# Kernel optimization log

Measured on AMD Instinct MI355X. Metric: run time of the kernel, lower is better.

Reference implementation:

```python
import jax, jax.numpy as jnp
import numpy as np
from jax import lax

DN = ('NCHW', 'OIHW', 'NCHW')


def _conv(x, w):
    # Conv2d(k=3, stride=2, padding=1, bias=False)
    return lax.conv_general_dilated(x, w, (2, 2), [(1, 1), (1, 1)], dimension_numbers=DN)


def _deconv(x, w):
    # ConvTranspose2d(k=3, stride=2, padding=1, output_padding=1, bias=False)
    # == input dilation 2 with asymmetric pad (k-1-p, k-1-p+output_padding) = (1, 2)
    return lax.conv_general_dilated(x, w, (1, 1), [(1, 2), (1, 2)], lhs_dilation=(2, 2), dimension_numbers=DN)


def _vq(z, codebook):
    B, C, H, W = z.shape
    z_flat = jnp.transpose(z, (0, 2, 3, 1)).reshape(-1, C)  # [BHW, C]
    dist = (jnp.sum(z_flat * z_flat, axis=1, keepdims=True)
            - 2.0 * z_flat @ codebook.T
            + jnp.sum(codebook * codebook, axis=1)[None, :])  # [BHW, K]
    ids = jnp.argmin(dist, axis=1)  # [BHW]
    e_k = codebook[ids]  # [BHW, C]
    e_k_st = z_flat + lax.stop_gradient(e_k - z_flat)
    e_k = jnp.transpose(e_k.reshape(B, H, W, C), (0, 3, 1, 2))
    e_k_st = jnp.transpose(e_k_st.reshape(B, H, W, C), (0, 3, 1, 2))
    return e_k, e_k_st, ids.reshape(B, H, W)


def _forward(x, enc_w0, enc_w1, enc_w2, codebook, dec_w0, dec_w1, dec_w2):
    # encoder
    h = jax.nn.relu(_conv(x, enc_w0))
    h = jax.nn.relu(_conv(h, enc_w1))
    z = _conv(h, enc_w2)  # no relu on last encoder layer
    # vector quantize
    e_k, e_k_st, ids = _vq(z, codebook)
    # decoder
    d = jax.nn.relu(_deconv(e_k_st, dec_w0))
    d = jax.nn.relu(_deconv(d, dec_w1))
    out = jax.nn.sigmoid(_deconv(d, dec_w2))
    return out, z, e_k, ids


def setup_inputs() -> dict:
    key = jax.random.key(0)
    ks = jax.random.split(key, 8)
    fan = lambda s: 1.0 / np.sqrt(np.prod(s[1:]))
    K = 1024
    return {
        'x': jax.random.uniform(ks[0], (32, 3, 256, 256), dtype=jnp.float32),
        'enc_w0': jax.random.normal(ks[1], (64, 3, 3, 3), jnp.float32) * fan((64, 3, 3, 3)),
        'enc_w1': jax.random.normal(ks[2], (128, 64, 3, 3), jnp.float32) * fan((128, 64, 3, 3)),
        'enc_w2': jax.random.normal(ks[3], (256, 128, 3, 3), jnp.float32) * fan((256, 128, 3, 3)),
        'codebook': jax.random.uniform(ks[4], (K, 256), jnp.float32, -1.0 / K, 1.0 / K),
        'dec_w0': jax.random.normal(ks[5], (128, 256, 3, 3), jnp.float32) * fan((128, 256, 3, 3)),
        'dec_w1': jax.random.normal(ks[6], (64, 128, 3, 3), jnp.float32) * fan((64, 128, 3, 3)),
        'dec_w2': jax.random.normal(ks[7], (3, 64, 3, 3), jnp.float32) * fan((3, 64, 3, 3)),
    }


def reference(x, enc_w0, enc_w1, enc_w2, codebook, dec_w0, dec_w1, dec_w2):
    return _forward(x, enc_w0, enc_w1, enc_w2, codebook, dec_w0, dec_w1, dec_w2)
```

## Files before the change

### kernel.cpp

```cpp
#include <hip/hip_runtime.h>
#include <math.h>


__global__ __launch_bounds__(256) void pad_zero_k(float* __restrict__ buf,
                                                  int HP, int WP) {
  float* p = buf + (size_t)blockIdx.x * HP * WP;
  const int tid = threadIdx.x;
  if (tid < WP) p[tid] = 0.f;
  if (tid >= 1 && tid < HP) p[(size_t)tid * WP] = 0.f;
}

template <int CIN, int COB, int PY, int LX, int MINW, int ACT>
__global__ __launch_bounds__(256, MINW) void conv3x3_s2_py(
    const float* __restrict__ in, const float* __restrict__ wgt,
    float* __restrict__ out, int COUT, int HIN, int WIN, int tilesW,
    int OHP, int OWP, int po) {
  const int HOUT = HIN >> 1, WOUT = WIN >> 1;
  const int YG = 256 / LX;
  const int tid = threadIdx.x;
  const int x = (blockIdx.x % tilesW) * LX + (tid % LX);
  const int y0 = (blockIdx.x / tilesW) * (YG * PY) + (tid / LX) * PY;
  const int co0 = blockIdx.y * COB;
  const int n = blockIdx.z;
  if (x >= WOUT || y0 >= HOUT) return;

  float acc[COB][PY], sum[COB][PY];
#pragma unroll
  for (int c = 0; c < COB; ++c)
#pragma unroll
    for (int r = 0; r < PY; ++r) { acc[c][r] = 0.f; sum[c][r] = 0.f; }

  const int ix0 = 2 * x - 1;
  const int iy0 = 2 * y0 - 1;
  for (int ci = 0; ci < CIN; ++ci) {
    const float* ip = in + (size_t)(n * CIN + ci) * HIN * WIN;
    float v[2 * PY + 1][3];
#pragma unroll
    for (int j = 0; j < 2 * PY + 1; ++j) {
      const int iy = iy0 + j;
      const bool yok = (unsigned)iy < (unsigned)HIN;
#pragma unroll
      for (int kx = 0; kx < 3; ++kx) {
        const int ix = ix0 + kx;
        v[j][kx] =
            (yok && (unsigned)ix < (unsigned)WIN) ? ip[iy * WIN + ix] : 0.f;
      }
    }
#pragma unroll
    for (int t = 0; t < 9; ++t) {
      const int kk = ci * 9 + t;
      if (CIN * 9 > 384 && (kk == 384 || kk == 768)) {
#pragma unroll
        for (int c = 0; c < COB; ++c)
#pragma unroll
          for (int r = 0; r < PY; ++r) {
            sum[c][r] = sum[c][r] + acc[c][r];
            acc[c][r] = 0.f;
          }
      }
      const int ky = t / 3, kx = t % 3;
#pragma unroll
      for (int c = 0; c < COB; ++c) {
        const float w = wgt[((size_t)(co0 + c) * CIN + ci) * 9 + t];
#pragma unroll
        for (int r = 0; r < PY; ++r)
          acc[c][r] = fmaf(v[2 * r + ky][kx], w, acc[c][r]);
      }
    }
  }
#pragma unroll
  for (int c = 0; c < COB; ++c)
#pragma unroll
    for (int r = 0; r < PY; ++r) {
      if (y0 + r < HOUT) {
        float rv = sum[c][r] + acc[c][r];
        if (ACT == 1) rv = fmaxf(rv, 0.f);
        out[(((size_t)n * COUT + co0 + c) * OHP + y0 + r + po) * OWP + x + po] =
            rv;
      }
    }
}

template <int CIN, int COB, int PY, int LX, int WINL, int MINW, int ACT,
          int PO>
__global__ __launch_bounds__(256, MINW) void conv3x3_s2_pad(
    const float* __restrict__ in, const float* __restrict__ wgt,
    float* __restrict__ out, int COUT, int tilesW) {
  constexpr int WP = WINL + 1;
  constexpr int HP = WINL + 1;
  constexpr size_t planeP = (size_t)HP * WP;
  constexpr int HOUT = WINL >> 1, WOUT = WINL >> 1;
  constexpr int OWP = WOUT + PO;
  constexpr int OHP = HOUT + PO;
  const int YG = 256 / LX;
  const int tid = threadIdx.x;
  const int x = (blockIdx.x % tilesW) * LX + (tid % LX);
  const int y0 = (blockIdx.x / tilesW) * (YG * PY) + (tid / LX) * PY;
  const int co0 = blockIdx.y * COB;
  const int n = blockIdx.z;
  if (x >= WOUT || y0 >= HOUT) return;

  float acc[COB][PY], sum[COB][PY];
#pragma unroll
  for (int c = 0; c < COB; ++c)
#pragma unroll
    for (int r = 0; r < PY; ++r) { acc[c][r] = 0.f; sum[c][r] = 0.f; }

  const float* bp = in + (size_t)(n * CIN) * planeP + (size_t)(2 * y0) * WP +
                    2 * x;
  for (int ci = 0; ci < CIN; ++ci, bp += planeP) {
    float v[2 * PY + 1][3];
#pragma unroll
    for (int j = 0; j < 2 * PY + 1; ++j)
#pragma unroll
      for (int kx = 0; kx < 3; ++kx) v[j][kx] = bp[j * WP + kx];
#pragma unroll
    for (int t = 0; t < 9; ++t) {
      const int kk = ci * 9 + t;
      if (CIN * 9 > 384 && (kk == 384 || kk == 768)) {
#pragma unroll
        for (int c = 0; c < COB; ++c)
#pragma unroll
          for (int r = 0; r < PY; ++r) {
            sum[c][r] = sum[c][r] + acc[c][r];
            acc[c][r] = 0.f;
          }
      }
      const int ky = t / 3, kx = t % 3;
#pragma unroll
      for (int c = 0; c < COB; ++c) {
        const float w = wgt[((size_t)(co0 + c) * CIN + ci) * 9 + t];
#pragma unroll
        for (int r = 0; r < PY; ++r)
          acc[c][r] = fmaf(v[2 * r + ky][kx], w, acc[c][r]);
      }
    }
  }
#pragma unroll
  for (int c = 0; c < COB; ++c)
#pragma unroll
    for (int r = 0; r < PY; ++r) {
      float rv = sum[c][r] + acc[c][r];
      if (ACT == 1) rv = fmaxf(rv, 0.f);
      out[(((size_t)n * COUT + co0 + c) * OHP + y0 + r + PO) * OWP + x + PO] =
          rv;
    }
}

template <int CIN, int COB, int MINW, int ACT>
__global__ __launch_bounds__(256, MINW) void deconv3x3_s2_quad2(
    const float* __restrict__ in, const float* __restrict__ wgt,
    float* __restrict__ out, int COUT, int HIN, int WIN, int tilesW) {
  const int HOUT = HIN * 2, WOUT = WIN * 2;
  const int tid = threadIdx.x;
  const int mx0 = ((blockIdx.x % tilesW) * 16 + (tid & 15)) * 2;
  const int my = (blockIdx.x / tilesW) * 16 + (tid >> 4);
  const int co0 = blockIdx.y * COB;
  const int n = blockIdx.z;
  if (mx0 >= WIN || my >= HIN) return;
  const bool xe = (mx0 + 2 < WIN);
  const bool ye = (my + 1 < HIN);

  float accA[COB][4], accB[COB][4];
#pragma unroll
  for (int c = 0; c < COB; ++c)
#pragma unroll
    for (int q = 0; q < 4; ++q) { accA[c][q] = 0.f; accB[c][q] = 0.f; }

  const size_t plane = (size_t)HIN * WIN;
  const float* ip = in + (size_t)(n * CIN) * plane + (size_t)my * WIN + mx0;
  for (int ci = 0; ci < CIN; ++ci, ip += plane) {
    const float v00 = ip[0];
    const float v01 = ip[1];
    const float v02 = xe ? ip[2] : 0.f;
    const float v10 = ye ? ip[WIN] : 0.f;
    const float v11 = ye ? ip[WIN + 1] : 0.f;
    const float v12 = (xe && ye) ? ip[WIN + 2] : 0.f;
#pragma unroll
    for (int c = 0; c < COB; ++c) {
      const float* w = wgt + ((size_t)(co0 + c) * CIN + ci) * 9;
      accA[c][0] = fmaf(v00, w[4], accA[c][0]);
      accA[c][1] = fmaf(v00, w[3], accA[c][1]);
      accA[c][1] = fmaf(v01, w[5], accA[c][1]);
      accA[c][2] = fmaf(v00, w[1], accA[c][2]);
      accA[c][2] = fmaf(v10, w[7], accA[c][2]);
      accA[c][3] = fmaf(v00, w[0], accA[c][3]);
      accA[c][3] = fmaf(v01, w[2], accA[c][3]);
      accA[c][3] = fmaf(v10, w[6], accA[c][3]);
      accA[c][3] = fmaf(v11, w[8], accA[c][3]);
      accB[c][0] = fmaf(v01, w[4], accB[c][0]);
      accB[c][1] = fmaf(v01, w[3], accB[c][1]);
      accB[c][1] = fmaf(v02, w[5], accB[c][1]);
      accB[c][2] = fmaf(v01, w[1], accB[c][2]);
      accB[c][2] = fmaf(v11, w[7], accB[c][2]);
      accB[c][3] = fmaf(v01, w[0], accB[c][3]);
      accB[c][3] = fmaf(v02, w[2], accB[c][3]);
      accB[c][3] = fmaf(v11, w[6], accB[c][3]);
      accB[c][3] = fmaf(v12, w[8], accB[c][3]);
    }
  }

  const int y0 = 2 * my, x0 = 2 * mx0;
#pragma unroll
  for (int c = 0; c < COB; ++c) {
    float rA[4], rB[4];
#pragma unroll
    for (int q = 0; q < 4; ++q) {
      float a = accA[c][q], b = accB[c][q];
      if (ACT == 1) { a = fmaxf(a, 0.f); b = fmaxf(b, 0.f); }
      if (ACT == 2) {
        a = 1.f / (1.f + expf(-a));
        b = 1.f / (1.f + expf(-b));
      }
      rA[q] = a; rB[q] = b;
    }
    float* op = out + (((size_t)n * COUT + co0 + c) * HOUT + y0) * WOUT + x0;
    float4 lo; lo.x = rA[0]; lo.y = rA[1]; lo.z = rB[0]; lo.w = rB[1];
    float4 hi; hi.x = rA[2]; hi.y = rA[3]; hi.z = rB[2]; hi.w = rB[3];
    *reinterpret_cast<float4*>(op) = lo;
    *reinterpret_cast<float4*>(op + WOUT) = hi;
  }
}

__global__ __launch_bounds__(256) void z2_np_k(const float* __restrict__ z,
                                               float* __restrict__ z2) {
#pragma clang fp contract(off)
  const int p = blockIdx.x * 256 + threadIdx.x;
  const int n = p >> 10, hw = p & 1023;
  const float* zb = z + (size_t)n * 262144 + hw;
  float blk[2];
#pragma unroll
  for (int b = 0; b < 2; ++b) {
    float r[8];
#pragma unroll
    for (int j = 0; j < 8; ++j) {
      const float v = zb[(size_t)(b * 128 + j) * 1024];
      r[j] = v * v;
    }
    for (int i = 8; i < 128; i += 8) {
#pragma unroll
      for (int j = 0; j < 8; ++j) {
        const float v = zb[(size_t)(b * 128 + i + j) * 1024];
        const float m = v * v;
        r[j] = r[j] + m;
      }
    }
    blk[b] = ((r[0] + r[1]) + (r[2] + r[3])) + ((r[4] + r[5]) + (r[6] + r[7]));
  }
  z2[p] = blk[0] + blk[1];
}

__global__ __launch_bounds__(256) void c2_np_k(const float* __restrict__ cb,
                                               float* __restrict__ c2) {
#pragma clang fp contract(off)
  const int jrow = blockIdx.x * 256 + threadIdx.x;
  const float* row = cb + (size_t)jrow * 256;
  float blk[2];
#pragma unroll
  for (int b = 0; b < 2; ++b) {
    float r[8];
#pragma unroll
    for (int j = 0; j < 8; ++j) {
      const float v = row[b * 128 + j];
      r[j] = v * v;
    }
    for (int i = 8; i < 128; i += 8) {
#pragma unroll
      for (int j = 0; j < 8; ++j) {
        const float v = row[b * 128 + i + j];
        const float m = v * v;
        r[j] = r[j] + m;
      }
    }
    blk[b] = ((r[0] + r[1]) + (r[2] + r[3])) + ((r[4] + r[5]) + (r[6] + r[7]));
  }
  c2[jrow] = blk[0] + blk[1];
}

__global__ __launch_bounds__(256) void vq_scores_part_k(
    const float* __restrict__ z, const float* __restrict__ cb,
    const float* __restrict__ z2, const float* __restrict__ c2,
    float* __restrict__ pdist, int* __restrict__ pid) {
  __shared__ float zS[32][64];
  __shared__ float cT[32][68];
  const int tid = threadIdx.x;
  const int p0 = blockIdx.x * 64;
  const int jb = blockIdx.y;
  const int n = p0 >> 10;
  const int hw0 = p0 & 1023;
  const float* zb = z + (size_t)n * 262144 + hw0;

  const int tp = tid >> 4;
  const int tj = tid & 15;

  const float4 z2q =
      *reinterpret_cast<const float4*>(&z2[p0 + tp * 4]);
  const float z2v[4] = {z2q.x, z2q.y, z2q.z, z2q.w};

  float run_d[4];
  int run_id[4];
#pragma unroll
  for (int ii = 0; ii < 4; ++ii) { run_d[ii] = 3.4e38f; run_id[ii] = 0; }

  for (int j0 = jb * 512; j0 < jb * 512 + 512; j0 += 64) {
    float acc[4][4];
#pragma unroll
    for (int a = 0; a < 4; ++a)
#pragma unroll
      for (int b = 0; b < 4; ++b) acc[a][b] = 0.f;

    for (int k0 = 0; k0 < 256; k0 += 32) {
      __syncthreads();
#pragma unroll
      for (int i = 0; i < 8; ++i) {
        const int q = i * 256 + tid;
        const int zc = q >> 6, zl = q & 63;
        zS[zc][zl] = zb[(size_t)(k0 + zc) * 1024 + zl];
        const int cw = q >> 5, cd = q & 31;
        cT[cd][cw] = cb[(size_t)(j0 + cw) * 256 + k0 + cd];
      }
      __syncthreads();
#pragma unroll
      for (int d = 0; d < 32; ++d) {
        const float4 zv = *reinterpret_cast<const float4*>(&zS[d][tp * 4]);
        const float4 cv = *reinterpret_cast<const float4*>(&cT[d][tj * 4]);
        acc[0][0] = fmaf(zv.x, cv.x, acc[0][0]);
        acc[0][1] = fmaf(zv.x, cv.y, acc[0][1]);
        acc[0][2] = fmaf(zv.x, cv.z, acc[0][2]);
        acc[0][3] = fmaf(zv.x, cv.w, acc[0][3]);
        acc[1][0] = fmaf(zv.y, cv.x, acc[1][0]);
        acc[1][1] = fmaf(zv.y, cv.y, acc[1][1]);
        acc[1][2] = fmaf(zv.y, cv.z, acc[1][2]);
        acc[1][3] = fmaf(zv.y, cv.w, acc[1][3]);
        acc[2][0] = fmaf(zv.z, cv.x, acc[2][0]);
        acc[2][1] = fmaf(zv.z, cv.y, acc[2][1]);
        acc[2][2] = fmaf(zv.z, cv.z, acc[2][2]);
        acc[2][3] = fmaf(zv.z, cv.w, acc[2][3]);
        acc[3][0] = fmaf(zv.w, cv.x, acc[3][0]);
        acc[3][1] = fmaf(zv.w, cv.y, acc[3][1]);
        acc[3][2] = fmaf(zv.w, cv.z, acc[3][2]);
        acc[3][3] = fmaf(zv.w, cv.w, acc[3][3]);
      }
    }

    {
#pragma clang fp contract(off)
      const float4 c2q =
          *reinterpret_cast<const float4*>(&c2[j0 + tj * 4]);
      const float c2a[4] = {c2q.x, c2q.y, c2q.z, c2q.w};
#pragma unroll
      for (int ii = 0; ii < 4; ++ii) {
#pragma unroll
        for (int jj = 0; jj < 4; ++jj) {
          const int j = j0 + tj * 4 + jj;
          const float m2 = 2.0f * acc[ii][jj];
          const float t1 = z2v[ii] + c2a[jj];
          const float dist = t1 - m2;
          if (dist < run_d[ii] || (dist == run_d[ii] && j < run_id[ii])) {
            run_d[ii] = dist;
            run_id[ii] = j;
          }
        }
      }
    }
  }

#pragma unroll
  for (int m = 1; m < 16; m <<= 1) {
#pragma unroll
    for (int ii = 0; ii < 4; ++ii) {
      const float od = __shfl_xor(run_d[ii], m, 64);
      const int oid = __shfl_xor(run_id[ii], m, 64);
      if (od < run_d[ii] || (od == run_d[ii] && oid < run_id[ii])) {
        run_d[ii] = od;
        run_id[ii] = oid;
      }
    }
  }
  if (tj == 0) {
#pragma unroll
    for (int ii = 0; ii < 4; ++ii) {
      pdist[jb * 32768 + p0 + tp * 4 + ii] = run_d[ii];
      pid[jb * 32768 + p0 + tp * 4 + ii] = run_id[ii];
    }
  }
}

__global__ __launch_bounds__(256) void vq_reduce_gather_k(
    const float* __restrict__ pdist, const int* __restrict__ pid,
    const float* __restrict__ cb, float* __restrict__ ek,
    float* __restrict__ ids) {
  const int p = blockIdx.x * 256 + threadIdx.x;
  float bd = pdist[p];
  int bi = pid[p];
  {
    const float od = pdist[32768 + p];
    const int oi = pid[32768 + p];
    if (od < bd || (od == bd && oi < bi)) { bd = od; bi = oi; }
  }
  ids[p] = (float)bi;
  const int n = p >> 10, hw = p & 1023;
  float* ekb = ek + (size_t)n * 262144 + hw;
  const float* cbr = cb + (size_t)bi * 256;
  for (int c = 0; c < 256; ++c) ekb[(size_t)c * 1024] = cbr[c];
}

extern "C" void kernel_launch(void* const* d_in, const int* in_sizes, int n_in,
                              void* d_out, int out_size, void* d_ws,
                              size_t ws_size, hipStream_t stream) {
  const float* x = (const float*)d_in[0];
  const float* enc_w0 = (const float*)d_in[1];
  const float* enc_w1 = (const float*)d_in[2];
  const float* enc_w2 = (const float*)d_in[3];
  const float* codebook = (const float*)d_in[4];
  const float* dec_w0 = (const float*)d_in[5];
  const float* dec_w1 = (const float*)d_in[6];
  const float* dec_w2 = (const float*)d_in[7];

  float* out = (float*)d_out;
  float* z_out = out + 6291456;
  float* ek_out = z_out + 8388608;
  float* ids_out = ek_out + 8388608;

  float* ws = (float*)d_ws;
  float* h1p = ws;
  float* h2p = ws + 34080768;
  float* d1 = h2p;
  float* d2 = h1p;
  float* s = ws + 51386368;
  float* z2 = s;
  float* c2 = s + 32768;
  float* pdist = s + 33792;
  int* pid = (int*)(s + 99328);

  pad_zero_k<<<32 * 64, 256, 0, stream>>>(h1p, 129, 129);
  pad_zero_k<<<32 * 128, 256, 0, stream>>>(h2p, 65, 65);

  conv3x3_s2_py<3, 8, 4, 16, 4, 1><<<dim3(16, 8, 32), 256, 0, stream>>>(
      x, enc_w0, h1p, 64, 256, 256, 8, 129, 129, 1);
  conv3x3_s2_pad<64, 8, 4, 16, 128, 4, 1, 1>
      <<<dim3(4, 16, 32), 256, 0, stream>>>(h1p, enc_w1, h2p, 128, 4);
  conv3x3_s2_pad<128, 8, 4, 32, 64, 4, 0, 0>
      <<<dim3(1, 32, 32), 256, 0, stream>>>(h2p, enc_w2, z_out, 256, 1);

  z2_np_k<<<128, 256, 0, stream>>>(z_out, z2);
  c2_np_k<<<4, 256, 0, stream>>>(codebook, c2);
  vq_scores_part_k<<<dim3(512, 2), 256, 0, stream>>>(z_out, codebook, z2, c2,
                                                     pdist, pid);
  vq_reduce_gather_k<<<128, 256, 0, stream>>>(pdist, pid, codebook, ek_out,
                                              ids_out);

  deconv3x3_s2_quad2<256, 8, 4, 1><<<dim3(2, 16, 32), 256, 0, stream>>>(
      ek_out, dec_w0, d1, 128, 32, 32, 1);
  deconv3x3_s2_quad2<128, 8, 4, 1><<<dim3(8, 8, 32), 256, 0, stream>>>(
      d1, dec_w1, d2, 64, 64, 64, 2);
  deconv3x3_s2_quad2<64, 3, 4, 2><<<dim3(32, 1, 32), 256, 0, stream>>>(
      d2, dec_w2, out, 3, 128, 128, 4);
}
```

Before: 1.564 ms.

## Stage conv and deconv weights in shared memory with register prefetch

The strided conv and transposed-conv kernels now copy each chunk of 32 input channels' weights for the block's output channels into LDS, using a register prefetch of the next chunk between barriers. The inner FMA loops read weights from LDS instead of global memory. The early-exit bounds checks are removed so every thread reaches the barriers; the current launch grids tile the outputs exactly. This trades the original wave-uniform global (likely scalar) weight loads for LDS broadcast reads plus block-wide synchronisation. That may not be cheaper and adds register and LDS pressure.

```diff
diff --git a/kernel.cpp b/kernel.cpp
--- a/kernel.cpp
+++ b/kernel.cpp
@@ -48,16 +48,6 @@
     }
 #pragma unroll
     for (int t = 0; t < 9; ++t) {
-      const int kk = ci * 9 + t;
-      if (CIN * 9 > 384 && (kk == 384 || kk == 768)) {
-#pragma unroll
-        for (int c = 0; c < COB; ++c)
-#pragma unroll
-          for (int r = 0; r < PY; ++r) {
-            sum[c][r] = sum[c][r] + acc[c][r];
-            acc[c][r] = 0.f;
-          }
-      }
       const int ky = t / 3, kx = t % 3;
 #pragma unroll
       for (int c = 0; c < COB; ++c) {
@@ -81,9 +71,9 @@
     }
 }
 
-template <int CIN, int COB, int PY, int LX, int WINL, int MINW, int ACT,
+template <int CIN, int COB, int PY, int LX, int WINL, int CHUNK, int ACT,
           int PO>
-__global__ __launch_bounds__(256, MINW) void conv3x3_s2_pad(
+__global__ __launch_bounds__(256, 4) void conv3x3_s2_pad_wlds(
     const float* __restrict__ in, const float* __restrict__ wgt,
     float* __restrict__ out, int COUT, int tilesW) {
   constexpr int WP = WINL + 1;
@@ -92,13 +82,16 @@
   constexpr int HOUT = WINL >> 1, WOUT = WINL >> 1;
   constexpr int OWP = WOUT + PO;
   constexpr int OHP = HOUT + PO;
+  constexpr int WTOT = COB * CHUNK * 9;
+  constexpr int NL = (WTOT + 255) / 256;
+  constexpr int NCH = CIN / CHUNK;
+  __shared__ float wS[WTOT];
   const int YG = 256 / LX;
   const int tid = threadIdx.x;
   const int x = (blockIdx.x % tilesW) * LX + (tid % LX);
   const int y0 = (blockIdx.x / tilesW) * (YG * PY) + (tid / LX) * PY;
   const int co0 = blockIdx.y * COB;
   const int n = blockIdx.z;
-  if (x >= WOUT || y0 >= HOUT) return;
 
   float acc[COB][PY], sum[COB][PY];
 #pragma unroll
@@ -108,31 +101,62 @@
 
   const float* bp = in + (size_t)(n * CIN) * planeP + (size_t)(2 * y0) * WP +
                     2 * x;
-  for (int ci = 0; ci < CIN; ++ci, bp += planeP) {
-    float v[2 * PY + 1][3];
-#pragma unroll
-    for (int j = 0; j < 2 * PY + 1; ++j)
-#pragma unroll
-      for (int kx = 0; kx < 3; ++kx) v[j][kx] = bp[j * WP + kx];
-#pragma unroll
-    for (int t = 0; t < 9; ++t) {
-      const int kk = ci * 9 + t;
-      if (CIN * 9 > 384 && (kk == 384 || kk == 768)) {
-#pragma unroll
-        for (int c = 0; c < COB; ++c)
-#pragma unroll
-          for (int r = 0; r < PY; ++r) {
-            sum[c][r] = sum[c][r] + acc[c][r];
-            acc[c][r] = 0.f;
-          }
-      }
-      const int ky = t / 3, kx = t % 3;
-#pragma unroll
-      for (int c = 0; c < COB; ++c) {
-        const float w = wgt[((size_t)(co0 + c) * CIN + ci) * 9 + t];
-#pragma unroll
-        for (int r = 0; r < PY; ++r)
-          acc[c][r] = fmaf(v[2 * r + ky][kx], w, acc[c][r]);
+
+  float rw[NL];
+#pragma unroll
+  for (int u = 0; u < NL; ++u) {
+    const int idx = u * 256 + tid;
+    if (idx < WTOT) {
+      const int c = idx / (CHUNK * 9), li = idx % (CHUNK * 9);
+      rw[u] = wgt[((size_t)(co0 + c) * CIN) * 9 + li];
+    }
+  }
+
+  for (int cc = 0; cc < NCH; ++cc) {
+    __syncthreads();
+#pragma unroll
+    for (int u = 0; u < NL; ++u) {
+      const int idx = u * 256 + tid;
+      if (idx < WTOT) wS[idx] = rw[u];
+    }
+    __syncthreads();
+    if (cc + 1 < NCH) {
+#pragma unroll
+      for (int u = 0; u < NL; ++u) {
+        const int idx = u * 256 + tid;
+        if (idx < WTOT) {
+          const int c = idx / (CHUNK * 9), li = idx % (CHUNK * 9);
+          rw[u] = wgt[((size_t)(co0 + c) * CIN + (cc + 1) * CHUNK) * 9 + li];
+        }
+      }
+    }
+    for (int ciq = 0; ciq < CHUNK; ++ciq, bp += planeP) {
+      const int ci = cc * CHUNK + ciq;
+      float v[2 * PY + 1][3];
+#pragma unroll
+      for (int j = 0; j < 2 * PY + 1; ++j)
+#pragma unroll
+        for (int kx = 0; kx < 3; ++kx) v[j][kx] = bp[j * WP + kx];
+#pragma unroll
+      for (int t = 0; t < 9; ++t) {
+        const int kk = ci * 9 + t;
+        if (CIN * 9 > 384 && (kk == 384 || kk == 768)) {
+#pragma unroll
+          for (int c = 0; c < COB; ++c)
+#pragma unroll
+            for (int r = 0; r < PY; ++r) {
+              sum[c][r] = sum[c][r] + acc[c][r];
+              acc[c][r] = 0.f;
+            }
+        }
+        const int ky = t / 3, kx = t % 3;
+#pragma unroll
+        for (int c = 0; c < COB; ++c) {
+          const float w = wS[(c * CHUNK + ciq) * 9 + t];
+#pragma unroll
+          for (int r = 0; r < PY; ++r)
+            acc[c][r] = fmaf(v[2 * r + ky][kx], w, acc[c][r]);
+        }
       }
     }
   }
@@ -147,17 +171,20 @@
     }
 }
 
-template <int CIN, int COB, int MINW, int ACT>
-__global__ __launch_bounds__(256, MINW) void deconv3x3_s2_quad2(
+template <int CIN, int COB, int CHUNK, int ACT>
+__global__ __launch_bounds__(256, 4) void deconv3x3_s2_wlds(
     const float* __restrict__ in, const float* __restrict__ wgt,
     float* __restrict__ out, int COUT, int HIN, int WIN, int tilesW) {
+  constexpr int WTOT = COB * CHUNK * 9;
+  constexpr int NL = (WTOT + 255) / 256;
+  constexpr int NCH = CIN / CHUNK;
+  __shared__ float wS[WTOT];
   const int HOUT = HIN * 2, WOUT = WIN * 2;
   const int tid = threadIdx.x;
   const int mx0 = ((blockIdx.x % tilesW) * 16 + (tid & 15)) * 2;
   const int my = (blockIdx.x / tilesW) * 16 + (tid >> 4);
   const int co0 = blockIdx.y * COB;
   const int n = blockIdx.z;
-  if (mx0 >= WIN || my >= HIN) return;
   const bool xe = (mx0 + 2 < WIN);
   const bool ye = (my + 1 < HIN);
 
@@ -169,34 +196,64 @@
 
   const size_t plane = (size_t)HIN * WIN;
   const float* ip = in + (size_t)(n * CIN) * plane + (size_t)my * WIN + mx0;
-  for (int ci = 0; ci < CIN; ++ci, ip += plane) {
-    const float v00 = ip[0];
-    const float v01 = ip[1];
-    const float v02 = xe ? ip[2] : 0.f;
-    const float v10 = ye ? ip[WIN] : 0.f;
-    const float v11 = ye ? ip[WIN + 1] : 0.f;
-    const float v12 = (xe && ye) ? ip[WIN + 2] : 0.f;
-#pragma unroll
-    for (int c = 0; c < COB; ++c) {
-      const float* w = wgt + ((size_t)(co0 + c) * CIN + ci) * 9;
-      accA[c][0] = fmaf(v00, w[4], accA[c][0]);
-      accA[c][1] = fmaf(v00, w[3], accA[c][1]);
-      accA[c][1] = fmaf(v01, w[5], accA[c][1]);
-      accA[c][2] = fmaf(v00, w[1], accA[c][2]);
-      accA[c][2] = fmaf(v10, w[7], accA[c][2]);
-      accA[c][3] = fmaf(v00, w[0], accA[c][3]);
-      accA[c][3] = fmaf(v01, w[2], accA[c][3]);
-      accA[c][3] = fmaf(v10, w[6], accA[c][3]);
-      accA[c][3] = fmaf(v11, w[8], accA[c][3]);
-      accB[c][0] = fmaf(v01, w[4], accB[c][0]);
-      accB[c][1] = fmaf(v01, w[3], accB[c][1]);
-      accB[c][1] = fmaf(v02, w[5], accB[c][1]);
-      accB[c][2] = fmaf(v01, w[1], accB[c][2]);
-      accB[c][2] = fmaf(v11, w[7], accB[c][2]);
-      accB[c][3] = fmaf(v01, w[0], accB[c][3]);
-      accB[c][3] = fmaf(v02, w[2], accB[c][3]);
-      accB[c][3] = fmaf(v11, w[6], accB[c][3]);
-      accB[c][3] = fmaf(v12, w[8], accB[c][3]);
+
+  float rw[NL];
+#pragma unroll
+  for (int u = 0; u < NL; ++u) {
+    const int idx = u * 256 + tid;
+    if (idx < WTOT) {
+      const int c = idx / (CHUNK * 9), li = idx % (CHUNK * 9);
+      rw[u] = wgt[((size_t)(co0 + c) * CIN) * 9 + li];
+    }
+  }
+
+  for (int cc = 0; cc < NCH; ++cc) {
+    __syncthreads();
+#pragma unroll
+    for (int u = 0; u < NL; ++u) {
+      const int idx = u * 256 + tid;
+      if (idx < WTOT) wS[idx] = rw[u];
+    }
+    __syncthreads();
+    if (cc + 1 < NCH) {
+#pragma unroll
+      for (int u = 0; u < NL; ++u) {
+        const int idx = u * 256 + tid;
+        if (idx < WTOT) {
+          const int c = idx / (CHUNK * 9), li = idx % (CHUNK * 9);
+          rw[u] = wgt[((size_t)(co0 + c) * CIN + (cc + 1) * CHUNK) * 9 + li];
+        }
+      }
+    }
+    for (int ciq = 0; ciq < CHUNK; ++ciq, ip += plane) {
+      const float v00 = ip[0];
+      const float v01 = ip[1];
+      const float v02 = xe ? ip[2] : 0.f;
+      const float v10 = ye ? ip[WIN] : 0.f;
+      const float v11 = ye ? ip[WIN + 1] : 0.f;
+      const float v12 = (xe && ye) ? ip[WIN + 2] : 0.f;
+#pragma unroll
+      for (int c = 0; c < COB; ++c) {
+        const float* w = &wS[(c * CHUNK + ciq) * 9];
+        accA[c][0] = fmaf(v00, w[4], accA[c][0]);
+        accA[c][1] = fmaf(v00, w[3], accA[c][1]);
+        accA[c][1] = fmaf(v01, w[5], accA[c][1]);
+        accA[c][2] = fmaf(v00, w[1], accA[c][2]);
+        accA[c][2] = fmaf(v10, w[7], accA[c][2]);
+        accA[c][3] = fmaf(v00, w[0], accA[c][3]);
+        accA[c][3] = fmaf(v01, w[2], accA[c][3]);
+        accA[c][3] = fmaf(v10, w[6], accA[c][3]);
+        accA[c][3] = fmaf(v11, w[8], accA[c][3]);
+        accB[c][0] = fmaf(v01, w[4], accB[c][0]);
+        accB[c][1] = fmaf(v01, w[3], accB[c][1]);
+        accB[c][1] = fmaf(v02, w[5], accB[c][1]);
+        accB[c][2] = fmaf(v01, w[1], accB[c][2]);
+        accB[c][2] = fmaf(v11, w[7], accB[c][2]);
+        accB[c][3] = fmaf(v01, w[0], accB[c][3]);
+        accB[c][3] = fmaf(v02, w[2], accB[c][3]);
+        accB[c][3] = fmaf(v11, w[6], accB[c][3]);
+        accB[c][3] = fmaf(v12, w[8], accB[c][3]);
+      }
     }
   }
 
@@ -438,9 +495,9 @@
 
   conv3x3_s2_py<3, 8, 4, 16, 4, 1><<<dim3(16, 8, 32), 256, 0, stream>>>(
       x, enc_w0, h1p, 64, 256, 256, 8, 129, 129, 1);
-  conv3x3_s2_pad<64, 8, 4, 16, 128, 4, 1, 1>
+  conv3x3_s2_pad_wlds<64, 8, 4, 16, 128, 32, 1, 1>
       <<<dim3(4, 16, 32), 256, 0, stream>>>(h1p, enc_w1, h2p, 128, 4);
-  conv3x3_s2_pad<128, 8, 4, 32, 64, 4, 0, 0>
+  conv3x3_s2_pad_wlds<128, 8, 4, 32, 64, 32, 0, 0>
       <<<dim3(1, 32, 32), 256, 0, stream>>>(h2p, enc_w2, z_out, 256, 1);
 
   z2_np_k<<<128, 256, 0, stream>>>(z_out, z2);
@@ -450,10 +507,10 @@
   vq_reduce_gather_k<<<128, 256, 0, stream>>>(pdist, pid, codebook, ek_out,
                                               ids_out);
 
-  deconv3x3_s2_quad2<256, 8, 4, 1><<<dim3(2, 16, 32), 256, 0, stream>>>(
+  deconv3x3_s2_wlds<256, 8, 32, 1><<<dim3(2, 16, 32), 256, 0, stream>>>(
       ek_out, dec_w0, d1, 128, 32, 32, 1);
-  deconv3x3_s2_quad2<128, 8, 4, 1><<<dim3(8, 8, 32), 256, 0, stream>>>(
+  deconv3x3_s2_wlds<128, 8, 32, 1><<<dim3(8, 8, 32), 256, 0, stream>>>(
       d1, dec_w1, d2, 64, 64, 64, 2);
-  deconv3x3_s2_quad2<64, 3, 4, 2><<<dim3(32, 1, 32), 256, 0, stream>>>(
+  deconv3x3_s2_wlds<64, 3, 32, 2><<<dim3(32, 1, 32), 256, 0, stream>>>(
       d2, dec_w2, out, 3, 128, 128, 4);
 }
```

Result: slower. 2.014 ms (+28.8%).
